# Kernel tuning notes

Hardware: AMD Instinct MI355X
Metric: run time of the kernel (lower is better)

The kernel has to match this reference:

```python
import jax, jax.numpy as jnp
import numpy as np

BATCH = 4096
LATENT = 2048
ZDIM = 128
TEMP = 0.5
PRIOR = 0.3
PRIOR_PRIME = 0.5
GAMMA = 1.0
BETA = 0.0
EPS = 1e-8  # torch CosineSimilarity eps


def setup_inputs() -> dict:
    key = jax.random.key(0)
    k = jax.random.split(key, 6)
    return {
        "h_i": jax.random.normal(k[0], (BATCH, LATENT), dtype=jnp.float32),
        "h_j": jax.random.normal(k[1], (BATCH, LATENT), dtype=jnp.float32),
        "z_i": jax.random.normal(k[2], (BATCH, ZDIM), dtype=jnp.float32),
        "z_j": jax.random.normal(k[3], (BATCH, ZDIM), dtype=jnp.float32),
        "target": jax.random.randint(k[4], (BATCH, 1), 0, 2, dtype=jnp.int64 if jax.config.jax_enable_x64 else jnp.int32),
        "W": jax.random.normal(k[5], (1, LATENT), dtype=jnp.float32) * (1.0 / np.sqrt(LATENT)),
        "b": jnp.zeros((1,), dtype=jnp.float32),
        "weight_onnpu": jnp.asarray(0.5, dtype=jnp.float32),
    }


def _onnpu_loss(inp, target):
    # inp: [B, 1] classifier logit; target: [B, 1] in {0, 1} -> {-1, +1}
    t = (target * 2 - 1).astype(inp.dtype)
    positive = (t == 1).astype(inp.dtype)
    unlabeled = (t == -1).astype(inp.dtype)
    one = jnp.asarray(1.0, inp.dtype)
    n_pos = jnp.maximum(one, jnp.sum(positive))
    n_unl = jnp.maximum(one, jnp.sum(unlabeled))
    sig = jax.nn.sigmoid  # loss(x) = sigmoid(-x)
    y_pos = sig(-(positive * inp)) * positive
    y_pos_inv = sig(positive * inp) * positive
    y_unl = sig(unlabeled * inp) * unlabeled
    positive_risk = PRIOR_PRIME / n_pos * jnp.sum(y_pos)
    negative_risk = ((1.0 - PRIOR_PRIME) / (n_unl * (1.0 - PRIOR)) * jnp.sum(y_unl)
                     - (1.0 - PRIOR_PRIME) * PRIOR / (n_pos * (1.0 - PRIOR)) * jnp.sum(y_pos_inv))
    # nnPU correction (nnPU=True, beta=0, gamma=1)
    return jnp.where(negative_risk < -BETA, -GAMMA * negative_risk,
                     positive_risk + negative_risk)


def _nt_xent_loss(z_i, z_j):
    B = z_i.shape[0]
    N = 2 * B
    z = jnp.concatenate([z_i, z_j], axis=0)  # [N, D]
    zn = z / jnp.maximum(jnp.linalg.norm(z, axis=1, keepdims=True), EPS)
    sim = (zn @ zn.T) / TEMP  # [N, N] cosine similarity / temperature
    idx = jnp.arange(N)
    pos = sim[idx, (idx + B) % N]  # positive pair logit per row
    # CE over [positive | all-other-than-self]: denominator is logsumexp over
    # the row with the self-similarity (diagonal) excluded.
    sim_masked = jnp.where(idx[:, None] == idx[None, :], -jnp.inf, sim)
    lse = jax.nn.logsumexp(sim_masked, axis=1)
    return jnp.sum(lse - pos) / N


def reference(h_i, h_j, z_i, z_j, target, W, b, weight_onnpu):
    logit_i = h_i @ W.T + b  # [B, 1]
    logit_j = h_j @ W.T + b
    onnpu_l = 0.5 * (_onnpu_loss(logit_i, target) + _onnpu_loss(logit_j, target))
    nt_xent_l = _nt_xent_loss(z_i, z_j)
    return weight_onnpu * onnpu_l + (1.0 - weight_onnpu) * nt_xent_l
```

## Files before the change

kernel.cpp:

```cpp
#include <hip/hip_runtime.h>

#define BATCH  4096
#define NROWS  8192
#define LATENT 2048
#define ZDIM   128
#define PRIORc       0.3f
#define PRIOR_PRIMEc 0.5f
#define ZSCALE 1.6986436f

typedef __attribute__((ext_vector_type(8))) short bf16x8;
typedef __attribute__((ext_vector_type(4))) float f32x4;

__device__ inline unsigned short f2bf_rne(float f) {
    unsigned int u = __float_as_uint(f);
    u = u + 0x7fffu + ((u >> 16) & 1u);
    return (unsigned short)(u >> 16);
}
__device__ inline float bf2f(unsigned short h) {
    return __uint_as_float(((unsigned int)h) << 16);
}
__device__ inline float wave_reduce_sum(float v) {
#pragma unroll
    for (int m = 1; m < 64; m <<= 1) v += __shfl_xor(v, m, 64);
    return v;
}

__global__ void k_zprep(const float* __restrict__ z_i, const float* __restrict__ z_j,
                        unsigned short* __restrict__ znb, float* __restrict__ pos,
                        float* __restrict__ expdiag, float* __restrict__ S_row) {
    int gid = blockIdx.x * 256 + threadIdx.x;
    if (gid < NROWS) S_row[gid] = 0.f;

    int wave = threadIdx.x >> 6, lane = threadIdx.x & 63;
    int r = blockIdx.x * 4 + wave;
    int p = r + BATCH;
    float2 a = ((const float2*)(z_i + (size_t)r * ZDIM))[lane];
    float2 c = ((const float2*)(z_j + (size_t)r * ZDIM))[lane];
    float sa = wave_reduce_sum(a.x * a.x + a.y * a.y);
    float sc = wave_reduce_sum(c.x * c.x + c.y * c.y);
    float dd = wave_reduce_sum(a.x * c.x + a.y * c.y);
    float inva = 1.f / fmaxf(sqrtf(sa), 1e-8f);
    float invc = 1.f / fmaxf(sqrtf(sc), 1e-8f);
    if (lane == 0) {
        float pv = 2.0f * dd * inva * invc;
        pos[r] = pv;
        pos[p] = pv;
    }
    int kt = lane >> 4;
    int q  = (lane >> 2) & 3;
    int j  = (lane & 3) * 2;
    int lrow = q * 16;
    float fa = inva * ZSCALE, fc = invc * ZSCALE;
    ushort2 wa, wc;
    wa.x = f2bf_rne(a.x * fa); wa.y = f2bf_rne(a.y * fa);
    wc.x = f2bf_rne(c.x * fc); wc.y = f2bf_rne(c.y * fc);
    {
        size_t off = ((size_t)((r >> 4) * 4 + kt) * 64 + (lrow + (r & 15))) * 8 + j;
        *(ushort2*)(znb + off) = wa;
    }
    {
        size_t off = ((size_t)((p >> 4) * 4 + kt) * 64 + (lrow + (p & 15))) * 8 + j;
        *(ushort2*)(znb + off) = wc;
    }
    float xa = bf2f(wa.x), ya = bf2f(wa.y);
    float xc = bf2f(wc.x), yc = bf2f(wc.y);
    float sda = wave_reduce_sum(xa * xa + ya * ya);
    float sdc = wave_reduce_sum(xc * xc + yc * yc);
    if (lane == 0) {
        expdiag[r] = __builtin_amdgcn_exp2f(sda);
        expdiag[p] = __builtin_amdgcn_exp2f(sdc);
    }
}

__global__ void __launch_bounds__(256, 3) k_mega(
        const unsigned short* __restrict__ znb, float* __restrict__ S_row,
        const float* __restrict__ h_i, const float* __restrict__ h_j,
        const float* __restrict__ W, const float* __restrict__ bb,
        float* __restrict__ logits) {
    int bid = blockIdx.x;
    int lane = threadIdx.x & 63, wave = threadIdx.x >> 6;
    if (bid < 1024) {
        int q = lane >> 4, t = lane & 15;
        int row0 = (bid & 63) * 128 + (wave >> 1) * 64;
        int gA = row0 >> 4;
        const bf16x8* zf = (const bf16x8*)znb;

        bf16x8 a[4][4];
#pragma unroll
        for (int mt = 0; mt < 4; ++mt)
#pragma unroll
            for (int kt = 0; kt < 4; ++kt)
                a[mt][kt] = zf[(size_t)((gA + mt) * 4 + kt) * 64 + lane];

        float s[16];
#pragma unroll
        for (int i = 0; i < 16; ++i) s[i] = 0.f;

        int colbase = (bid >> 6) * 512 + (wave & 1) * 64;
        int cb4 = colbase >> 4;
        bf16x8 b[4];
#pragma unroll
        for (int kt = 0; kt < 4; ++kt)
            b[kt] = zf[(size_t)(cb4 * 4 + kt) * 64 + lane];

        f32x4 zero = {0.f, 0.f, 0.f, 0.f};
#pragma unroll 1
        for (int it = 0; it < 4; ++it) {
#pragma unroll
            for (int nt = 0; nt < 4; ++nt) {
                bf16x8 bn[4];
                if (!(it == 3 && nt == 3)) {
                    int ng = cb4 + (nt == 3 ? (it + 1) * 8 : it * 8 + nt + 1);
#pragma unroll
                    for (int kt = 0; kt < 4; ++kt)
                        bn[kt] = zf[(size_t)(ng * 4 + kt) * 64 + lane];
                }
                f32x4 acc[4];
#pragma unroll
                for (int mt = 0; mt < 4; ++mt)
                    acc[mt] = __builtin_amdgcn_mfma_f32_16x16x32_bf16(a[mt][0], b[0], zero, 0, 0, 0);
#pragma unroll
                for (int kt = 1; kt < 4; ++kt)
#pragma unroll
                    for (int mt = 0; mt < 4; ++mt)
                        acc[mt] = __builtin_amdgcn_mfma_f32_16x16x32_bf16(a[mt][kt], b[kt], acc[mt], 0, 0, 0);
#pragma unroll
                for (int mt = 0; mt < 4; ++mt)
#pragma unroll
                    for (int reg = 0; reg < 4; ++reg)
                        s[mt * 4 + reg] += __builtin_amdgcn_exp2f(acc[mt][reg]);
#pragma unroll
                for (int kt = 0; kt < 4; ++kt) b[kt] = bn[kt];
            }
        }
#pragma unroll
        for (int i = 0; i < 16; ++i) {
            float v = s[i];
            v += __shfl_xor(v, 1, 64);
            v += __shfl_xor(v, 2, 64);
            v += __shfl_xor(v, 4, 64);
            v += __shfl_xor(v, 8, 64);
            if (t == 0) atomicAdd(&S_row[row0 + (i >> 2) * 16 + q * 4 + (i & 3)], v);
        }
    } else {
        int r = (bid - 1024) * 4 + wave;
        const float* h = (r < BATCH) ? (h_i + (size_t)r * LATENT)
                                     : (h_j + (size_t)(r - BATCH) * LATENT);
        const f32x4* h4 = (const f32x4*)h;
        const f32x4* w4 = (const f32x4*)W;
        float s = 0.f;
#pragma unroll
        for (int itr = 0; itr < 8; ++itr) {
            f32x4 av = __builtin_nontemporal_load(&h4[itr * 64 + lane]);
            f32x4 wv = w4[itr * 64 + lane];
            s += av.x * wv.x + av.y * wv.y + av.z * wv.z + av.w * wv.w;
        }
        s = wave_reduce_sum(s);
        if (lane == 0) logits[r] = s + bb[0];
    }
}

__global__ void k_final(const float* __restrict__ S_row, const float* __restrict__ pos,
                        const float* __restrict__ expdiag,
                        const float* __restrict__ logits, const int* __restrict__ target,
                        const float* __restrict__ w_onnpu, float* __restrict__ out) {
    float nt_s = 0.f;
    for (int r = threadIdx.x; r < NROWS; r += 1024)
        nt_s += __logf(S_row[r] - expdiag[r]) - pos[r];
    float v[8];
#pragma unroll
    for (int i = 0; i < 8; ++i) v[i] = 0.f;
    for (int r = threadIdx.x; r < BATCH; r += 1024) {
        float li = logits[r], lj = logits[BATCH + r];
        bool p = (target[r] == 1);
        float si_n = 1.f / (1.f + __expf(li));
        float si_p = 1.f / (1.f + __expf(-li));
        float sj_n = 1.f / (1.f + __expf(lj));
        float sj_p = 1.f / (1.f + __expf(-lj));
        v[0] += p ? 1.f : 0.f;
        v[1] += p ? 0.f : 1.f;
        v[2] += p ? si_n : 0.f;
        v[3] += p ? si_p : 0.f;
        v[4] += p ? 0.f : si_p;
        v[5] += p ? sj_n : 0.f;
        v[6] += p ? sj_p : 0.f;
        v[7] += p ? 0.f : sj_p;
    }
    __shared__ float red[16][9];
    int wave = threadIdx.x >> 6, lane = threadIdx.x & 63;
    nt_s = wave_reduce_sum(nt_s);
#pragma unroll
    for (int i = 0; i < 8; ++i) v[i] = wave_reduce_sum(v[i]);
    if (lane == 0) {
        red[wave][0] = nt_s;
#pragma unroll
        for (int i = 0; i < 8; ++i) red[wave][1 + i] = v[i];
    }
    __syncthreads();
    if (threadIdx.x == 0) {
        float t[9];
#pragma unroll
        for (int i = 0; i < 9; ++i) {
            float acc = 0.f;
#pragma unroll
            for (int wv = 0; wv < 16; ++wv) acc += red[wv][i];
            t[i] = acc;
        }
        float ntxent = t[0] / (float)NROWS;
        float np = fmaxf(1.f, t[1]), nu = fmaxf(1.f, t[2]);
        float pr_i = PRIOR_PRIMEc / np * t[3];
        float nr_i = (1.f - PRIOR_PRIMEc) / (nu * (1.f - PRIORc)) * t[5]
                   - (1.f - PRIOR_PRIMEc) * PRIORc / (np * (1.f - PRIORc)) * t[4];
        float li_loss = (nr_i < 0.f) ? -nr_i : (pr_i + nr_i);
        float pr_j = PRIOR_PRIMEc / np * t[6];
        float nr_j = (1.f - PRIOR_PRIMEc) / (nu * (1.f - PRIORc)) * t[8]
                   - (1.f - PRIOR_PRIMEc) * PRIORc / (np * (1.f - PRIORc)) * t[7];
        float lj_loss = (nr_j < 0.f) ? -nr_j : (pr_j + nr_j);
        float onnpu = 0.5f * (li_loss + lj_loss);
        float w = w_onnpu[0];
        out[0] = w * onnpu + (1.f - w) * ntxent;
    }
}

extern "C" void kernel_launch(void* const* d_in, const int* in_sizes, int n_in,
                              void* d_out, int out_size, void* d_ws, size_t ws_size,
                              hipStream_t stream) {
    const float* h_i = (const float*)d_in[0];
    const float* h_j = (const float*)d_in[1];
    const float* z_i = (const float*)d_in[2];
    const float* z_j = (const float*)d_in[3];
    const int* target = (const int*)d_in[4];
    const float* W = (const float*)d_in[5];
    const float* b = (const float*)d_in[6];
    const float* w_onnpu = (const float*)d_in[7];

    char* ws = (char*)d_ws;
    unsigned short* znb = (unsigned short*)ws;
    float* S_row   = (float*)(ws + 2097152);
    float* pos     = (float*)(ws + 2097152 + 32768);
    float* logits  = (float*)(ws + 2097152 + 65536);
    float* expdiag = (float*)(ws + 2097152 + 98304);
    float* out = (float*)d_out;

    k_zprep<<<1024, 256, 0, stream>>>(z_i, z_j, znb, pos, expdiag, S_row);
    k_mega<<<3072, 256, 0, stream>>>(znb, S_row, h_i, h_j, W, b, logits);
    k_final<<<1, 1024, 0, stream>>>(S_row, pos, expdiag, logits, target, w_onnpu, out);
}
```

Baseline: 144.6 us.

## Exploit similarity matrix symmetry and move logit GEMV into prep kernel

The similarity kernel now computes only upper-triangular 16x16 tiles of the symmetric Gram matrix. Each exp tile is added to both the row sums and, through column reductions, the transposed rows' sums, which roughly halves the MFMA and exp work. The h·W logit GEMV moves out of the similarity kernel into the z-prep kernel, so it overlaps with normalization instead. The cost is extra atomics for the column sums, half-empty early-exit blocks in a 2D grid, and branch divergence from the diagonal masking.

```diff
diff --git a/kernel.cpp b/kernel.cpp
--- a/kernel.cpp
+++ b/kernel.cpp
@@ -25,122 +25,55 @@
     return v;
 }
 
-__global__ void k_zprep(const float* __restrict__ z_i, const float* __restrict__ z_j,
-                        unsigned short* __restrict__ znb, float* __restrict__ pos,
-                        float* __restrict__ expdiag, float* __restrict__ S_row) {
-    int gid = blockIdx.x * 256 + threadIdx.x;
-    if (gid < NROWS) S_row[gid] = 0.f;
-
+__global__ void k_prep(const float* __restrict__ z_i, const float* __restrict__ z_j,
+                       unsigned short* __restrict__ znb, float* __restrict__ pos,
+                       float* __restrict__ expdiag, float* __restrict__ S_row,
+                       const float* __restrict__ h_i, const float* __restrict__ h_j,
+                       const float* __restrict__ W, const float* __restrict__ bb,
+                       float* __restrict__ logits) {
+    int bid = blockIdx.x;
     int wave = threadIdx.x >> 6, lane = threadIdx.x & 63;
-    int r = blockIdx.x * 4 + wave;
-    int p = r + BATCH;
-    float2 a = ((const float2*)(z_i + (size_t)r * ZDIM))[lane];
-    float2 c = ((const float2*)(z_j + (size_t)r * ZDIM))[lane];
-    float sa = wave_reduce_sum(a.x * a.x + a.y * a.y);
-    float sc = wave_reduce_sum(c.x * c.x + c.y * c.y);
-    float dd = wave_reduce_sum(a.x * c.x + a.y * c.y);
-    float inva = 1.f / fmaxf(sqrtf(sa), 1e-8f);
-    float invc = 1.f / fmaxf(sqrtf(sc), 1e-8f);
-    if (lane == 0) {
-        float pv = 2.0f * dd * inva * invc;
-        pos[r] = pv;
-        pos[p] = pv;
-    }
-    int kt = lane >> 4;
-    int q  = (lane >> 2) & 3;
-    int j  = (lane & 3) * 2;
-    int lrow = q * 16;
-    float fa = inva * ZSCALE, fc = invc * ZSCALE;
-    ushort2 wa, wc;
-    wa.x = f2bf_rne(a.x * fa); wa.y = f2bf_rne(a.y * fa);
-    wc.x = f2bf_rne(c.x * fc); wc.y = f2bf_rne(c.y * fc);
-    {
-        size_t off = ((size_t)((r >> 4) * 4 + kt) * 64 + (lrow + (r & 15))) * 8 + j;
-        *(ushort2*)(znb + off) = wa;
-    }
-    {
-        size_t off = ((size_t)((p >> 4) * 4 + kt) * 64 + (lrow + (p & 15))) * 8 + j;
-        *(ushort2*)(znb + off) = wc;
-    }
-    float xa = bf2f(wa.x), ya = bf2f(wa.y);
-    float xc = bf2f(wc.x), yc = bf2f(wc.y);
-    float sda = wave_reduce_sum(xa * xa + ya * ya);
-    float sdc = wave_reduce_sum(xc * xc + yc * yc);
-    if (lane == 0) {
-        expdiag[r] = __builtin_amdgcn_exp2f(sda);
-        expdiag[p] = __builtin_amdgcn_exp2f(sdc);
-    }
-}
-
-__global__ void __launch_bounds__(256, 3) k_mega(
-        const unsigned short* __restrict__ znb, float* __restrict__ S_row,
-        const float* __restrict__ h_i, const float* __restrict__ h_j,
-        const float* __restrict__ W, const float* __restrict__ bb,
-        float* __restrict__ logits) {
-    int bid = blockIdx.x;
-    int lane = threadIdx.x & 63, wave = threadIdx.x >> 6;
     if (bid < 1024) {
-        int q = lane >> 4, t = lane & 15;
-        int row0 = (bid & 63) * 128 + (wave >> 1) * 64;
-        int gA = row0 >> 4;
-        const bf16x8* zf = (const bf16x8*)znb;
-
-        bf16x8 a[4][4];
-#pragma unroll
-        for (int mt = 0; mt < 4; ++mt)
-#pragma unroll
-            for (int kt = 0; kt < 4; ++kt)
-                a[mt][kt] = zf[(size_t)((gA + mt) * 4 + kt) * 64 + lane];
-
-        float s[16];
-#pragma unroll
-        for (int i = 0; i < 16; ++i) s[i] = 0.f;
-
-        int colbase = (bid >> 6) * 512 + (wave & 1) * 64;
-        int cb4 = colbase >> 4;
-        bf16x8 b[4];
-#pragma unroll
-        for (int kt = 0; kt < 4; ++kt)
-            b[kt] = zf[(size_t)(cb4 * 4 + kt) * 64 + lane];
-
-        f32x4 zero = {0.f, 0.f, 0.f, 0.f};
-#pragma unroll 1
-        for (int it = 0; it < 4; ++it) {
-#pragma unroll
-            for (int nt = 0; nt < 4; ++nt) {
-                bf16x8 bn[4];
-                if (!(it == 3 && nt == 3)) {
-                    int ng = cb4 + (nt == 3 ? (it + 1) * 8 : it * 8 + nt + 1);
-#pragma unroll
-                    for (int kt = 0; kt < 4; ++kt)
-                        bn[kt] = zf[(size_t)(ng * 4 + kt) * 64 + lane];
-                }
-                f32x4 acc[4];
-#pragma unroll
-                for (int mt = 0; mt < 4; ++mt)
-                    acc[mt] = __builtin_amdgcn_mfma_f32_16x16x32_bf16(a[mt][0], b[0], zero, 0, 0, 0);
-#pragma unroll
-                for (int kt = 1; kt < 4; ++kt)
-#pragma unroll
-                    for (int mt = 0; mt < 4; ++mt)
-                        acc[mt] = __builtin_amdgcn_mfma_f32_16x16x32_bf16(a[mt][kt], b[kt], acc[mt], 0, 0, 0);
-#pragma unroll
-                for (int mt = 0; mt < 4; ++mt)
-#pragma unroll
-                    for (int reg = 0; reg < 4; ++reg)
-                        s[mt * 4 + reg] += __builtin_amdgcn_exp2f(acc[mt][reg]);
-#pragma unroll
-                for (int kt = 0; kt < 4; ++kt) b[kt] = bn[kt];
-            }
-        }
-#pragma unroll
-        for (int i = 0; i < 16; ++i) {
-            float v = s[i];
-            v += __shfl_xor(v, 1, 64);
-            v += __shfl_xor(v, 2, 64);
-            v += __shfl_xor(v, 4, 64);
-            v += __shfl_xor(v, 8, 64);
-            if (t == 0) atomicAdd(&S_row[row0 + (i >> 2) * 16 + q * 4 + (i & 3)], v);
+        int gid = bid * 256 + threadIdx.x;
+        if (gid < NROWS) S_row[gid] = 0.f;
+
+        int r = bid * 4 + wave;
+        int p = r + BATCH;
+        float2 a = ((const float2*)(z_i + (size_t)r * ZDIM))[lane];
+        float2 c = ((const float2*)(z_j + (size_t)r * ZDIM))[lane];
+        float sa = wave_reduce_sum(a.x * a.x + a.y * a.y);
+        float sc = wave_reduce_sum(c.x * c.x + c.y * c.y);
+        float dd = wave_reduce_sum(a.x * c.x + a.y * c.y);
+        float inva = 1.f / fmaxf(sqrtf(sa), 1e-8f);
+        float invc = 1.f / fmaxf(sqrtf(sc), 1e-8f);
+        if (lane == 0) {
+            float pv = 2.0f * dd * inva * invc;
+            pos[r] = pv;
+            pos[p] = pv;
+        }
+        int kt = lane >> 4;
+        int q  = (lane >> 2) & 3;
+        int j  = (lane & 3) * 2;
+        int lrow = q * 16;
+        float fa = inva * ZSCALE, fc = invc * ZSCALE;
+        ushort2 wa, wc;
+        wa.x = f2bf_rne(a.x * fa); wa.y = f2bf_rne(a.y * fa);
+        wc.x = f2bf_rne(c.x * fc); wc.y = f2bf_rne(c.y * fc);
+        {
+            size_t off = ((size_t)((r >> 4) * 4 + kt) * 64 + (lrow + (r & 15))) * 8 + j;
+            *(ushort2*)(znb + off) = wa;
+        }
+        {
+            size_t off = ((size_t)((p >> 4) * 4 + kt) * 64 + (lrow + (p & 15))) * 8 + j;
+            *(ushort2*)(znb + off) = wc;
+        }
+        float xa = bf2f(wa.x), ya = bf2f(wa.y);
+        float xc = bf2f(wc.x), yc = bf2f(wc.y);
+        float sda = wave_reduce_sum(xa * xa + ya * ya);
+        float sdc = wave_reduce_sum(xc * xc + yc * yc);
+        if (lane == 0) {
+            expdiag[r] = __builtin_amdgcn_exp2f(sda);
+            expdiag[p] = __builtin_amdgcn_exp2f(sdc);
         }
     } else {
         int r = (bid - 1024) * 4 + wave;
@@ -157,6 +90,87 @@
         }
         s = wave_reduce_sum(s);
         if (lane == 0) logits[r] = s + bb[0];
+    }
+}
+
+__global__ void __launch_bounds__(256, 3) k_sim(const unsigned short* __restrict__ znb,
+                                                float* __restrict__ S_row) {
+    int bx = blockIdx.x, by = blockIdx.y;
+    if (bx * 32 + 31 < by * 8) return;
+    int lane = threadIdx.x & 63, wave = threadIdx.x >> 6;
+    int q = lane >> 4, t = lane & 15;
+    int gA = by * 8 + (wave >> 1) * 4;
+    int base16 = bx * 32 + (wave & 1) * 4;
+    const bf16x8* zf = (const bf16x8*)znb;
+
+    bf16x8 a[4][4];
+#pragma unroll
+    for (int mt = 0; mt < 4; ++mt)
+#pragma unroll
+        for (int kt = 0; kt < 4; ++kt)
+            a[mt][kt] = zf[(size_t)((gA + mt) * 4 + kt) * 64 + lane];
+
+    float s[16];
+#pragma unroll
+    for (int i = 0; i < 16; ++i) s[i] = 0.f;
+
+    bf16x8 b[4];
+#pragma unroll
+    for (int kt = 0; kt < 4; ++kt)
+        b[kt] = zf[(size_t)(base16 * 4 + kt) * 64 + lane];
+
+    f32x4 zero = {0.f, 0.f, 0.f, 0.f};
+#pragma unroll 1
+    for (int idx = 0; idx < 16; ++idx) {
+        int g_c = base16 + (idx >> 2) * 8 + (idx & 3);
+        bf16x8 bn[4];
+        if (idx < 15) {
+            int ng = base16 + ((idx + 1) >> 2) * 8 + ((idx + 1) & 3);
+#pragma unroll
+            for (int kt = 0; kt < 4; ++kt)
+                bn[kt] = zf[(size_t)(ng * 4 + kt) * 64 + lane];
+        }
+        if (g_c >= gA) {
+            f32x4 acc[4];
+#pragma unroll
+            for (int mt = 0; mt < 4; ++mt)
+                acc[mt] = __builtin_amdgcn_mfma_f32_16x16x32_bf16(a[mt][0], b[0], zero, 0, 0, 0);
+#pragma unroll
+            for (int kt = 1; kt < 4; ++kt)
+#pragma unroll
+                for (int mt = 0; mt < 4; ++mt)
+                    acc[mt] = __builtin_amdgcn_mfma_f32_16x16x32_bf16(a[mt][kt], b[kt], acc[mt], 0, 0, 0);
+            float ecol = 0.f;
+#pragma unroll
+            for (int mt = 0; mt < 4; ++mt) {
+                bool rowv = (g_c >= gA + mt);
+                bool colv = (g_c >  gA + mt);
+                float em = 0.f;
+#pragma unroll
+                for (int reg = 0; reg < 4; ++reg) {
+                    float e = __builtin_amdgcn_exp2f(acc[mt][reg]);
+                    s[mt * 4 + reg] += rowv ? e : 0.f;
+                    em += e;
+                }
+                ecol += colv ? em : 0.f;
+            }
+            if (g_c > gA) {
+                ecol += __shfl_xor(ecol, 16, 64);
+                ecol += __shfl_xor(ecol, 32, 64);
+                if (lane < 16) atomicAdd(&S_row[g_c * 16 + lane], ecol);
+            }
+        }
+#pragma unroll
+        for (int kt = 0; kt < 4; ++kt) b[kt] = bn[kt];
+    }
+#pragma unroll
+    for (int i = 0; i < 16; ++i) {
+        float v = s[i];
+        v += __shfl_xor(v, 1, 64);
+        v += __shfl_xor(v, 2, 64);
+        v += __shfl_xor(v, 4, 64);
+        v += __shfl_xor(v, 8, 64);
+        if (t == 0) atomicAdd(&S_row[gA * 16 + (i >> 2) * 16 + q * 4 + (i & 3)], v);
     }
 }
 
@@ -242,7 +256,9 @@
     float* expdiag = (float*)(ws + 2097152 + 98304);
     float* out = (float*)d_out;
 
-    k_zprep<<<1024, 256, 0, stream>>>(z_i, z_j, znb, pos, expdiag, S_row);
-    k_mega<<<3072, 256, 0, stream>>>(znb, S_row, h_i, h_j, W, b, logits);
+    k_prep<<<3072, 256, 0, stream>>>(z_i, z_j, znb, pos, expdiag, S_row,
+                                     h_i, h_j, W, b, logits);
+    dim3 g(16, 64);
+    k_sim<<<g, 256, 0, stream>>>(znb, S_row);
     k_final<<<1, 1024, 0, stream>>>(S_row, pos, expdiag, logits, target, w_onnpu, out);
 }
```

New measurement: 157.2 us. 1.09x slower.
